# Kernel optimization log

Hardware: AMD Instinct MI355X
Metric: run time of the kernel (lower is better)

Reference implementation:

```python
import jax, jax.numpy as jnp
import numpy as np

B, S, D, H = 2, 2048, 1024, 16
DK = D // H  # 64


def setup_inputs() -> dict:
    key = jax.random.key(0)
    ks = jax.random.split(key, 9)
    query = jax.random.normal(ks[0], (B, S, D), dtype=jnp.float32)
    k_in = jax.random.normal(ks[1], (B, S, D), dtype=jnp.float32)
    v_in = jax.random.normal(ks[2], (B, S, D), dtype=jnp.float32)
    mask = jax.random.randint(ks[3], (B, S, S), 0, 2, dtype=jnp.int32)
    sc = 1.0 / np.sqrt(D)
    Wq = jax.random.normal(ks[4], (H, D, DK), dtype=jnp.float32) * sc  # per-head q proj
    Wk = jax.random.normal(ks[5], (H, D, DK), dtype=jnp.float32) * sc
    Wv = jax.random.normal(ks[6], (H, D, DK), dtype=jnp.float32) * sc
    Wu = jax.random.normal(ks[7], (D, D), dtype=jnp.float32) * sc  # unifyheads weight
    bu = jax.random.normal(ks[8], (D,), dtype=jnp.float32) * 0.01
    return {"query": query, "key": k_in, "value": v_in, "mask": mask,
            "Wq": Wq, "Wk": Wk, "Wv": Wv, "Wu": Wu, "bu": bu}


def reference(query, key, value, mask, Wq, Wk, Wv, Wu, bu):
    scale = DK ** 0.25  # original divides q and k each by d_k^(1/4)
    q = jnp.einsum('bsd,hdk->bhsk', query, Wq) / scale
    k = jnp.einsum('bsd,hdk->bhsk', key, Wk) / scale
    v = jnp.einsum('bsd,hdk->bhsk', value, Wv)
    scores = jnp.einsum('bhsk,bhtk->bhst', q, k)  # [B,H,S,S]
    scores = jnp.where(mask[:, None, :, :] == 0, jnp.float32(-1e9), scores)
    attn = jax.nn.softmax(scores, axis=-1)
    out = jnp.einsum('bhst,bhtk->bhsk', attn, v)
    out = jnp.transpose(out, (0, 2, 1, 3)).reshape(query.shape[0], query.shape[1], D)  # concat heads
    return out @ Wu + bu
```

## Files before the change

### kernel.cpp

```cpp
#include <hip/hip_runtime.h>
#include <hip/hip_bf16.h>


typedef __bf16 bf16_t;
typedef __attribute__((ext_vector_type(8))) __bf16 bf16x8;
typedef __attribute__((ext_vector_type(4))) float f32x4;
typedef unsigned int u32;

#define B_ 2
#define S_ 2048
#define D_ 1024
#define H_ 16
#define DK_ 64
#define NX_ (4096 * 1024)

static __device__ __forceinline__ f32x4 mfma16(bf16x8 a, bf16x8 b, f32x4 c) {
  return __builtin_amdgcn_mfma_f32_16x16x32_bf16(a, b, c, 0, 0, 0);
}

static __device__ __forceinline__ void async16(const bf16_t* g, bf16_t* l) {
  __builtin_amdgcn_global_load_lds(
      (const __attribute__((address_space(1))) u32*)g,
      (__attribute__((address_space(3))) u32*)l, 16, 0, 0);
}

__global__ __launch_bounds__(256) void cvt_x(const float* __restrict__ q,
                                             const float* __restrict__ k,
                                             const float* __restrict__ v,
                                             bf16_t* __restrict__ qo,
                                             bf16_t* __restrict__ ko,
                                             bf16_t* __restrict__ vo) {
  const int z = blockIdx.y;
  const float* src = (z == 0) ? q : (z == 1) ? k : v;
  bf16_t* dst = (z == 0) ? qo : (z == 1) ? ko : vo;
  size_t i = ((size_t)blockIdx.x * 256 + threadIdx.x) * 8;
  float4 a = *(const float4*)(src + i);
  float4 b = *(const float4*)(src + i + 4);
  bf16x8 o;
  o[0] = (bf16_t)a.x; o[1] = (bf16_t)a.y; o[2] = (bf16_t)a.z; o[3] = (bf16_t)a.w;
  o[4] = (bf16_t)b.x; o[5] = (bf16_t)b.y; o[6] = (bf16_t)b.z; o[7] = (bf16_t)b.w;
  *(bf16x8*)(dst + i) = o;
}

__global__ __launch_bounds__(256) void wtrans(
    const float* __restrict__ Wq, const float* __restrict__ Wk,
    const float* __restrict__ Wv, const float* __restrict__ Wu,
    bf16_t* __restrict__ Bq, bf16_t* __restrict__ Bk,
    bf16_t* __restrict__ Bv, bf16_t* __restrict__ Bu, float qkscale) {
  __shared__ __align__(16) bf16_t T[64][72];
  const int z = blockIdx.z;
  const float* W = (z == 0) ? Wq : (z == 1) ? Wk : (z == 2) ? Wv : Wu;
  bf16_t* BT = (z == 0) ? Bq : (z == 1) ? Bk : (z == 2) ? Bv : Bu;
  const float scale = (z <= 1) ? qkscale : 1.0f;
  const int d0 = blockIdx.x * 64, nt = blockIdx.y;
  const int tid = threadIdx.x;
  const int r = tid & 63, g = tid >> 6;

  const float* src = (z < 3)
      ? W + ((size_t)nt * D_ + d0 + r) * DK_ + g * 16
      : W + (size_t)(d0 + r) * D_ + nt * 64 + g * 16;
#pragma unroll
  for (int j = 0; j < 4; ++j) {
    float4 w4 = *(const float4*)(src + j * 4);
    T[g * 16 + j * 4 + 0][r] = (bf16_t)(w4.x * scale);
    T[g * 16 + j * 4 + 1][r] = (bf16_t)(w4.y * scale);
    T[g * 16 + j * 4 + 2][r] = (bf16_t)(w4.z * scale);
    T[g * 16 + j * 4 + 3][r] = (bf16_t)(w4.w * scale);
  }
  __syncthreads();
  const int orow = tid >> 3, seg = tid & 7;
#pragma unroll
  for (int p = 0; p < 2; ++p) {
    int rr = p * 32 + orow;
    *(bf16x8*)(BT + (size_t)(nt * 64 + rr) * D_ + d0 + seg * 8) =
        *(const bf16x8*)&T[rr][seg * 8];
  }
}

__global__ __launch_bounds__(256) void vt_build(const bf16_t* __restrict__ V,
                                                bf16_t* __restrict__ Vt) {
  __shared__ __align__(16) bf16_t T[64][72];
  const int r0 = blockIdx.x * 64;
  const int c0 = blockIdx.y * 64;
  const int tid = threadIdx.x;
#pragma unroll
  for (int it = 0; it < 2; ++it) {
    int t = tid + it * 256;
    int rr = t >> 3, cc = (t & 7) * 8;
    *(bf16x8*)&T[rr][cc] = *(const bf16x8*)(V + (size_t)(r0 + rr) * D_ + c0 + cc);
  }
  __syncthreads();
#pragma unroll
  for (int it = 0; it < 2; ++it) {
    int t = tid + it * 256;
    int cr = t >> 3, rc = (t & 7) * 8;
    bf16x8 v;
#pragma unroll
    for (int j = 0; j < 8; ++j) v[j] = T[rc + j][cr];
    *(bf16x8*)(Vt + (size_t)(c0 + cr) * 4096 + r0 + rc) = v;
  }
}

__global__ __launch_bounds__(256) void mask_pack(const int* __restrict__ mask,
                                                 unsigned int* __restrict__ bits) {
  int w = blockIdx.x * 256 + threadIdx.x;
  const int4* p = (const int4*)(mask + (size_t)w * 32);
  unsigned int v = 0;
#pragma unroll
  for (int i = 0; i < 8; ++i) {
    int4 m4 = p[i];
    v |= (m4.x != 0 ? 1u : 0u) << (i * 4 + 0);
    v |= (m4.y != 0 ? 1u : 0u) << (i * 4 + 1);
    v |= (m4.z != 0 ? 1u : 0u) << (i * 4 + 2);
    v |= (m4.w != 0 ? 1u : 0u) << (i * 4 + 3);
  }
  bits[w] = v;
}

template <bool BIAS_F32>
__global__ __launch_bounds__(256) void gemm_bt(
    const bf16_t* __restrict__ A0, const bf16_t* __restrict__ A1,
    const bf16_t* __restrict__ A2, const bf16_t* __restrict__ BT0,
    const bf16_t* __restrict__ BT1, const bf16_t* __restrict__ BT2,
    void* __restrict__ C0, void* __restrict__ C1, void* __restrict__ C2,
    const float* __restrict__ bias) {
  __shared__ __align__(16) bf16_t As[128 * 64];
  __shared__ __align__(16) bf16_t Bs[128 * 64];

  const int z = blockIdx.z;
  const bf16_t* A = (z == 0) ? A0 : (z == 1) ? A1 : A2;
  const bf16_t* BT = (z == 0) ? BT0 : (z == 1) ? BT1 : BT2;
  void* C = (z == 0) ? C0 : (z == 1) ? C1 : C2;

  const int tid = threadIdx.x;
  const int lane = tid & 63, wave = tid >> 6;
  const int l = lane & 15, quad = lane >> 4;
  const int wm = wave >> 1, wn = wave & 1;
  const int row0 = blockIdx.x * 128, col0 = blockIdx.y * 128;

  const int lr = lane >> 3;
  const int gc8 = (lane & 7) ^ lr;
  const int xl = l & 7;

  f32x4 acc[4][4];
#pragma unroll
  for (int i = 0; i < 4; ++i)
#pragma unroll
    for (int j = 0; j < 4; ++j) acc[i][j] = {0.f, 0.f, 0.f, 0.f};

  for (int k0 = 0; k0 < 1024; k0 += 64) {
    __syncthreads();
#pragma unroll
    for (int c = 0; c < 4; ++c) {
      int r = wave * 32 + c * 8;
      async16(A + (size_t)(row0 + r + lr) * 1024 + k0 + gc8 * 8, As + r * 64);
      async16(BT + (size_t)(col0 + r + lr) * 1024 + k0 + gc8 * 8, Bs + r * 64);
    }
    __syncthreads();

#pragma unroll
    for (int kh = 0; kh < 2; ++kh) {
      bf16x8 af[4], bf[4];
#pragma unroll
      for (int f = 0; f < 4; ++f)
        af[f] = *(const bf16x8*)&As[(wm * 64 + f * 16 + l) * 64 +
                                    (((kh * 4 + quad) ^ xl) * 8)];
#pragma unroll
      for (int f = 0; f < 4; ++f)
        bf[f] = *(const bf16x8*)&Bs[(wn * 64 + f * 16 + l) * 64 +
                                    (((kh * 4 + quad) ^ xl) * 8)];
#pragma unroll
      for (int fm = 0; fm < 4; ++fm)
#pragma unroll
        for (int fn = 0; fn < 4; ++fn)
          acc[fm][fn] = mfma16(af[fm], bf[fn], acc[fm][fn]);
    }
  }

#pragma unroll
  for (int fm = 0; fm < 4; ++fm)
#pragma unroll
    for (int fn = 0; fn < 4; ++fn)
#pragma unroll
      for (int reg = 0; reg < 4; ++reg) {
        int row = row0 + wm * 64 + fm * 16 + quad * 4 + reg;
        int col = col0 + wn * 64 + fn * 16 + l;
        if (BIAS_F32)
          ((float*)C)[(size_t)row * 1024 + col] = acc[fm][fn][reg] + bias[col];
        else
          ((bf16_t*)C)[(size_t)row * 1024 + col] = (bf16_t)acc[fm][fn][reg];
      }
}

__global__ __launch_bounds__(256) void attn_kernel(
    const bf16_t* __restrict__ Qx, const bf16_t* __restrict__ Kx,
    const bf16_t* __restrict__ Vt, const unsigned int* __restrict__ mbits,
    bf16_t* __restrict__ out) {
  __shared__ __align__(16) bf16_t Ks[64 * 64];
  __shared__ __align__(16) bf16_t Vts[64 * 64];
  __shared__ __align__(16) bf16_t Ps[4][32][72];

  const int tid = threadIdx.x;
  const int lane = tid & 63, wave = tid >> 6;
  const int l = lane & 15, quad = lane >> 4;
  const int qt = blockIdx.x, h = blockIdx.y, b = blockIdx.z;
  const int ch = h * 64;
  const size_t rb = (size_t)b * S_;
  const int q0 = qt * 128 + wave * 32;

  const int lr = lane >> 3;
  const int gc8 = (lane & 7) ^ lr;
  const int xl = l & 7;

  bf16x8 aq[2][2];
#pragma unroll
  for (int mf = 0; mf < 2; ++mf) {
    const bf16_t* qp = Qx + (rb + q0 + mf * 16 + l) * D_ + ch;
    aq[mf][0] = *(const bf16x8*)(qp + quad * 8);
    aq[mf][1] = *(const bf16x8*)(qp + 32 + quad * 8);
  }

  const f32x4 zero = {0.f, 0.f, 0.f, 0.f};
  f32x4 o[2][4];
  float lpart[2][4];
#pragma unroll
  for (int mf = 0; mf < 2; ++mf)
#pragma unroll
    for (int i = 0; i < 4; ++i) { o[mf][i] = zero; lpart[mf][i] = 0.f; }

  for (int t0 = 0; t0 < S_; t0 += 64) {
    __syncthreads();
#pragma unroll
    for (int it = 0; it < 2; ++it) {
      int r0 = it * 32 + wave * 8;
      async16(Kx + (rb + t0 + r0 + lr) * D_ + ch + gc8 * 8, Ks + r0 * 64);
      async16(Vt + (size_t)(ch + r0 + lr) * 4096 + rb + t0 + gc8 * 8,
              Vts + r0 * 64);
    }
    __syncthreads();

    f32x4 sf[2][4];
#pragma unroll
    for (int ts = 0; ts < 4; ++ts) {
      int rK = (ts * 16 + l) * 64;
      bf16x8 bk0 = *(const bf16x8*)&Ks[rK + ((quad ^ xl) * 8)];
      bf16x8 bk1 = *(const bf16x8*)&Ks[rK + (((4 + quad) ^ xl) * 8)];
#pragma unroll
      for (int mf = 0; mf < 2; ++mf) {
        f32x4 c = mfma16(aq[mf][0], bk0, zero);
        sf[mf][ts] = mfma16(aq[mf][1], bk1, c);
      }
    }

#pragma unroll
    for (int mf = 0; mf < 2; ++mf)
#pragma unroll
      for (int reg = 0; reg < 4; ++reg) {
        int srow = q0 + mf * 16 + quad * 4 + reg;
        const u32* mp = mbits + (size_t)(b * S_ + srow) * (S_ / 32) + (t0 >> 5);
        u32 w0 = mp[0], w1 = mp[1];
#pragma unroll
        for (int ts = 0; ts < 4; ++ts) {
          u32 w = (ts < 2) ? w0 : w1;
          int bit = (ts & 1) * 16 + l;
          float keep = (float)((w >> bit) & 1u);
          float p = __expf(fminf(sf[mf][ts][reg], 30.0f)) * keep;
          lpart[mf][reg] += p;
          Ps[wave][mf * 16 + quad * 4 + reg][ts * 16 + l] = (bf16_t)p;
        }
      }

    bf16x8 ap[2][2];
#pragma unroll
    for (int mf = 0; mf < 2; ++mf) {
      ap[mf][0] = *(const bf16x8*)&Ps[wave][mf * 16 + l][quad * 8];
      ap[mf][1] = *(const bf16x8*)&Ps[wave][mf * 16 + l][32 + quad * 8];
    }
#pragma unroll
    for (int nt = 0; nt < 4; ++nt) {
      int rV = (nt * 16 + l) * 64;
      bf16x8 bv0 = *(const bf16x8*)&Vts[rV + ((quad ^ xl) * 8)];
      bf16x8 bv1 = *(const bf16x8*)&Vts[rV + (((4 + quad) ^ xl) * 8)];
#pragma unroll
      for (int mf = 0; mf < 2; ++mf) {
        o[mf][nt] = mfma16(ap[mf][0], bv0, o[mf][nt]);
        o[mf][nt] = mfma16(ap[mf][1], bv1, o[mf][nt]);
      }
    }
  }

#pragma unroll
  for (int mf = 0; mf < 2; ++mf)
#pragma unroll
    for (int reg = 0; reg < 4; ++reg) {
      float rsum = lpart[mf][reg];
#pragma unroll
      for (int m = 1; m < 16; m <<= 1) rsum += __shfl_xor(rsum, m);
      float inv = (rsum > 0.f) ? (1.f / rsum) : 0.f;
      int srow = q0 + mf * 16 + quad * 4 + reg;
      bf16_t* op = out + (rb + srow) * D_ + ch;
#pragma unroll
      for (int nt = 0; nt < 4; ++nt)
        op[nt * 16 + l] = (bf16_t)(o[mf][nt][reg] * inv);
    }
}

extern "C" void kernel_launch(void* const* d_in, const int* in_sizes, int n_in,
                              void* d_out, int out_size, void* d_ws, size_t ws_size,
                              hipStream_t stream) {
  const float* q_in = (const float*)d_in[0];
  const float* k_in = (const float*)d_in[1];
  const float* v_in = (const float*)d_in[2];
  const int* mask = (const int*)d_in[3];
  const float* Wq = (const float*)d_in[4];
  const float* Wk = (const float*)d_in[5];
  const float* Wv = (const float*)d_in[6];
  const float* Wu = (const float*)d_in[7];
  const float* bu = (const float*)d_in[8];
  float* outp = (float*)d_out;

  bf16_t* qx = (bf16_t*)d_ws;
  bf16_t* kx = qx + NX_;
  bf16_t* vx = kx + NX_;
  bf16_t* qb = vx + NX_;
  bf16_t* kb = qb + NX_;
  bf16_t* vb = kb + NX_;
  bf16_t* BTq = vb + NX_;
  bf16_t* BTk = BTq + D_ * D_;
  bf16_t* BTv = BTk + D_ * D_;
  bf16_t* BTu = BTv + D_ * D_;
  unsigned int* mb = (unsigned int*)(BTu + D_ * D_);
  bf16_t* ab = qx;
  bf16_t* vtb = kx;

  const float qkscale = 0.35355339059327373f;

  dim3 blk(256);
  cvt_x<<<dim3(2048, 3), blk, 0, stream>>>(q_in, k_in, v_in, qx, kx, vx);
  wtrans<<<dim3(16, 16, 4), blk, 0, stream>>>(Wq, Wk, Wv, Wu, BTq, BTk, BTv, BTu, qkscale);
  mask_pack<<<dim3(1024), blk, 0, stream>>>(mask, mb);
  gemm_bt<false><<<dim3(32, 8, 3), blk, 0, stream>>>(qx, kx, vx, BTq, BTk, BTv,
                                                     qb, kb, vb, nullptr);
  vt_build<<<dim3(64, 16), blk, 0, stream>>>(vb, vtb);
  attn_kernel<<<dim3(S_ / 128, H_, B_), blk, 0, stream>>>(qb, kb, vtb, mb, ab);
  gemm_bt<true><<<dim3(32, 8, 1), blk, 0, stream>>>(ab, ab, ab, BTu, BTu, BTu,
                                                    outp, outp, outp, bu);
}
```

Baseline: 298.5 us.

## Transpose score MFMA, shrink attention blocks, use 64-row tiles for output GEMM

The attention kernel now computes S^T by swapping the MFMA operands, so each lane holds four consecutive keys for one query row. That lets it read one mask nibble per lane, write P to LDS as packed bf16x4, and keep one running sum per row group. Attention blocks drop to 128 threads covering 64 queries, doubling the grid to raise occupancy and CU coverage. The output projection gets its own 64x128-tile GEMM kernel, giving it twice as many blocks. The cost is more K/V tile reloads per query and smaller GEMM tiles with less reuse.

```diff
diff --git a/kernel.cpp b/kernel.cpp
--- a/kernel.cpp
+++ b/kernel.cpp
@@ -3,6 +3,7 @@
 
 
 typedef __bf16 bf16_t;
+typedef __attribute__((ext_vector_type(4))) __bf16 bf16x4;
 typedef __attribute__((ext_vector_type(8))) __bf16 bf16x8;
 typedef __attribute__((ext_vector_type(4))) float f32x4;
 typedef unsigned int u32;
@@ -117,20 +118,18 @@
   bits[w] = v;
 }
 
-template <bool BIAS_F32>
 __global__ __launch_bounds__(256) void gemm_bt(
     const bf16_t* __restrict__ A0, const bf16_t* __restrict__ A1,
     const bf16_t* __restrict__ A2, const bf16_t* __restrict__ BT0,
     const bf16_t* __restrict__ BT1, const bf16_t* __restrict__ BT2,
-    void* __restrict__ C0, void* __restrict__ C1, void* __restrict__ C2,
-    const float* __restrict__ bias) {
+    bf16_t* __restrict__ C0, bf16_t* __restrict__ C1, bf16_t* __restrict__ C2) {
   __shared__ __align__(16) bf16_t As[128 * 64];
   __shared__ __align__(16) bf16_t Bs[128 * 64];
 
   const int z = blockIdx.z;
   const bf16_t* A = (z == 0) ? A0 : (z == 1) ? A1 : A2;
   const bf16_t* BT = (z == 0) ? BT0 : (z == 1) ? BT1 : BT2;
-  void* C = (z == 0) ? C0 : (z == 1) ? C1 : C2;
+  bf16_t* C = (z == 0) ? C0 : (z == 1) ? C1 : C2;
 
   const int tid = threadIdx.x;
   const int lane = tid & 63, wave = tid >> 6;
@@ -185,20 +184,83 @@
       for (int reg = 0; reg < 4; ++reg) {
         int row = row0 + wm * 64 + fm * 16 + quad * 4 + reg;
         int col = col0 + wn * 64 + fn * 16 + l;
-        if (BIAS_F32)
-          ((float*)C)[(size_t)row * 1024 + col] = acc[fm][fn][reg] + bias[col];
-        else
-          ((bf16_t*)C)[(size_t)row * 1024 + col] = (bf16_t)acc[fm][fn][reg];
+        C[(size_t)row * 1024 + col] = (bf16_t)acc[fm][fn][reg];
       }
 }
 
-__global__ __launch_bounds__(256) void attn_kernel(
+__global__ __launch_bounds__(256) void gemm_bt64(
+    const bf16_t* __restrict__ A, const bf16_t* __restrict__ BT,
+    float* __restrict__ C, const float* __restrict__ bias) {
+  __shared__ __align__(16) bf16_t As[64 * 64];
+  __shared__ __align__(16) bf16_t Bs[128 * 64];
+
+  const int tid = threadIdx.x;
+  const int lane = tid & 63, wave = tid >> 6;
+  const int l = lane & 15, quad = lane >> 4;
+  const int row0 = blockIdx.x * 64, col0 = blockIdx.y * 128;
+
+  const int lr = lane >> 3;
+  const int gc8 = (lane & 7) ^ lr;
+  const int xl = l & 7;
+
+  f32x4 acc[4][2];
+#pragma unroll
+  for (int i = 0; i < 4; ++i)
+#pragma unroll
+    for (int j = 0; j < 2; ++j) acc[i][j] = {0.f, 0.f, 0.f, 0.f};
+
+  for (int k0 = 0; k0 < 1024; k0 += 64) {
+    __syncthreads();
+#pragma unroll
+    for (int c = 0; c < 2; ++c) {
+      int r = wave * 16 + c * 8;
+      async16(A + (size_t)(row0 + r + lr) * 1024 + k0 + gc8 * 8, As + r * 64);
+    }
+#pragma unroll
+    for (int c = 0; c < 4; ++c) {
+      int r = wave * 32 + c * 8;
+      async16(BT + (size_t)(col0 + r + lr) * 1024 + k0 + gc8 * 8, Bs + r * 64);
+    }
+    __syncthreads();
+
+#pragma unroll
+    for (int kh = 0; kh < 2; ++kh) {
+      bf16x8 af[4], bf[2];
+#pragma unroll
+      for (int f = 0; f < 4; ++f)
+        af[f] = *(const bf16x8*)&As[(f * 16 + l) * 64 +
+                                    (((kh * 4 + quad) ^ xl) * 8)];
+#pragma unroll
+      for (int f = 0; f < 2; ++f)
+        bf[f] = *(const bf16x8*)&Bs[(wave * 32 + f * 16 + l) * 64 +
+                                    (((kh * 4 + quad) ^ xl) * 8)];
+#pragma unroll
+      for (int fm = 0; fm < 4; ++fm)
+#pragma unroll
+        for (int fn = 0; fn < 2; ++fn)
+          acc[fm][fn] = mfma16(af[fm], bf[fn], acc[fm][fn]);
+    }
+  }
+
+#pragma unroll
+  for (int fm = 0; fm < 4; ++fm)
+#pragma unroll
+    for (int fn = 0; fn < 2; ++fn)
+#pragma unroll
+      for (int reg = 0; reg < 4; ++reg) {
+        int row = row0 + fm * 16 + quad * 4 + reg;
+        int col = col0 + wave * 32 + fn * 16 + l;
+        C[(size_t)row * 1024 + col] = acc[fm][fn][reg] + bias[col];
+      }
+}
+
+__global__ __launch_bounds__(128) void attn_kernel(
     const bf16_t* __restrict__ Qx, const bf16_t* __restrict__ Kx,
     const bf16_t* __restrict__ Vt, const unsigned int* __restrict__ mbits,
     bf16_t* __restrict__ out) {
   __shared__ __align__(16) bf16_t Ks[64 * 64];
   __shared__ __align__(16) bf16_t Vts[64 * 64];
-  __shared__ __align__(16) bf16_t Ps[4][32][72];
+  __shared__ __align__(16) bf16_t Ps[2][32][72];
 
   const int tid = threadIdx.x;
   const int lane = tid & 63, wave = tid >> 6;
@@ -206,69 +268,69 @@
   const int qt = blockIdx.x, h = blockIdx.y, b = blockIdx.z;
   const int ch = h * 64;
   const size_t rb = (size_t)b * S_;
-  const int q0 = qt * 128 + wave * 32;
+  const int q0 = qt * 64 + wave * 32;
 
   const int lr = lane >> 3;
   const int gc8 = (lane & 7) ^ lr;
   const int xl = l & 7;
 
-  bf16x8 aq[2][2];
+  bf16x8 bq[2][2];
 #pragma unroll
   for (int mf = 0; mf < 2; ++mf) {
     const bf16_t* qp = Qx + (rb + q0 + mf * 16 + l) * D_ + ch;
-    aq[mf][0] = *(const bf16x8*)(qp + quad * 8);
-    aq[mf][1] = *(const bf16x8*)(qp + 32 + quad * 8);
+    bq[mf][0] = *(const bf16x8*)(qp + quad * 8);
+    bq[mf][1] = *(const bf16x8*)(qp + 32 + quad * 8);
   }
 
   const f32x4 zero = {0.f, 0.f, 0.f, 0.f};
   f32x4 o[2][4];
-  float lpart[2][4];
+  float lsum[2] = {0.f, 0.f};
 #pragma unroll
   for (int mf = 0; mf < 2; ++mf)
 #pragma unroll
-    for (int i = 0; i < 4; ++i) { o[mf][i] = zero; lpart[mf][i] = 0.f; }
+    for (int nt = 0; nt < 4; ++nt) o[mf][nt] = zero;
+
+  const u32* mrow[2];
+#pragma unroll
+  for (int mf = 0; mf < 2; ++mf)
+    mrow[mf] = mbits + (size_t)(b * S_ + q0 + mf * 16 + l) * (S_ / 32);
 
   for (int t0 = 0; t0 < S_; t0 += 64) {
     __syncthreads();
 #pragma unroll
-    for (int it = 0; it < 2; ++it) {
-      int r0 = it * 32 + wave * 8;
+    for (int it = 0; it < 4; ++it) {
+      int r0 = it * 16 + wave * 8;
       async16(Kx + (rb + t0 + r0 + lr) * D_ + ch + gc8 * 8, Ks + r0 * 64);
       async16(Vt + (size_t)(ch + r0 + lr) * 4096 + rb + t0 + gc8 * 8,
               Vts + r0 * 64);
     }
     __syncthreads();
 
-    f32x4 sf[2][4];
-#pragma unroll
-    for (int ts = 0; ts < 4; ++ts) {
-      int rK = (ts * 16 + l) * 64;
-      bf16x8 bk0 = *(const bf16x8*)&Ks[rK + ((quad ^ xl) * 8)];
-      bf16x8 bk1 = *(const bf16x8*)&Ks[rK + (((4 + quad) ^ xl) * 8)];
-#pragma unroll
-      for (int mf = 0; mf < 2; ++mf) {
-        f32x4 c = mfma16(aq[mf][0], bk0, zero);
-        sf[mf][ts] = mfma16(aq[mf][1], bk1, c);
+#pragma unroll
+    for (int mf = 0; mf < 2; ++mf) {
+      u32 mw0 = mrow[mf][(t0 >> 5)];
+      u32 mw1 = mrow[mf][(t0 >> 5) + 1];
+#pragma unroll
+      for (int ts = 0; ts < 4; ++ts) {
+        int rK = (ts * 16 + l) * 64;
+        bf16x8 ak0 = *(const bf16x8*)&Ks[rK + ((quad ^ xl) * 8)];
+        bf16x8 ak1 = *(const bf16x8*)&Ks[rK + (((4 + quad) ^ xl) * 8)];
+        f32x4 s = mfma16(ak0, bq[mf][0], zero);
+        s = mfma16(ak1, bq[mf][1], s);
+
+        u32 mw = (ts < 2) ? mw0 : mw1;
+        u32 nib = (mw >> ((ts & 1) * 16 + quad * 4)) & 0xFu;
+        bf16x4 pv;
+#pragma unroll
+        for (int reg = 0; reg < 4; ++reg) {
+          float e = __expf(fminf(s[reg], 30.0f));
+          float p = ((nib >> reg) & 1u) ? e : 0.0f;
+          lsum[mf] += p;
+          pv[reg] = (bf16_t)p;
+        }
+        *(bf16x4*)&Ps[wave][mf * 16 + l][ts * 16 + quad * 4] = pv;
       }
     }
-
-#pragma unroll
-    for (int mf = 0; mf < 2; ++mf)
-#pragma unroll
-      for (int reg = 0; reg < 4; ++reg) {
-        int srow = q0 + mf * 16 + quad * 4 + reg;
-        const u32* mp = mbits + (size_t)(b * S_ + srow) * (S_ / 32) + (t0 >> 5);
-        u32 w0 = mp[0], w1 = mp[1];
-#pragma unroll
-        for (int ts = 0; ts < 4; ++ts) {
-          u32 w = (ts < 2) ? w0 : w1;
-          int bit = (ts & 1) * 16 + l;
-          float keep = (float)((w >> bit) & 1u);
-          float p = __expf(fminf(sf[mf][ts][reg], 30.0f)) * keep;
-          lpart[mf][reg] += p;
-          Ps[wave][mf * 16 + quad * 4 + reg][ts * 16 + l] = (bf16_t)p;
-        }
-      }
 
     bf16x8 ap[2][2];
 #pragma unroll
@@ -290,19 +352,23 @@
   }
 
 #pragma unroll
-  for (int mf = 0; mf < 2; ++mf)
+  for (int mf = 0; mf < 2; ++mf) {
+    float rsum = lsum[mf];
+    rsum += __shfl_xor(rsum, 16);
+    rsum += __shfl_xor(rsum, 32);
+    float inv = (rsum > 0.f) ? (1.f / rsum) : 0.f;
+    float invr[4];
+#pragma unroll
+    for (int reg = 0; reg < 4; ++reg) invr[reg] = __shfl(inv, quad * 4 + reg);
 #pragma unroll
     for (int reg = 0; reg < 4; ++reg) {
-      float rsum = lpart[mf][reg];
-#pragma unroll
-      for (int m = 1; m < 16; m <<= 1) rsum += __shfl_xor(rsum, m);
-      float inv = (rsum > 0.f) ? (1.f / rsum) : 0.f;
       int srow = q0 + mf * 16 + quad * 4 + reg;
       bf16_t* op = out + (rb + srow) * D_ + ch;
 #pragma unroll
       for (int nt = 0; nt < 4; ++nt)
-        op[nt * 16 + l] = (bf16_t)(o[mf][nt][reg] * inv);
-    }
+        op[nt * 16 + l] = (bf16_t)(o[mf][nt][reg] * invr[reg]);
+    }
+  }
 }
 
 extern "C" void kernel_launch(void* const* d_in, const int* in_sizes, int n_in,
@@ -339,10 +405,9 @@
   cvt_x<<<dim3(2048, 3), blk, 0, stream>>>(q_in, k_in, v_in, qx, kx, vx);
   wtrans<<<dim3(16, 16, 4), blk, 0, stream>>>(Wq, Wk, Wv, Wu, BTq, BTk, BTv, BTu, qkscale);
   mask_pack<<<dim3(1024), blk, 0, stream>>>(mask, mb);
-  gemm_bt<false><<<dim3(32, 8, 3), blk, 0, stream>>>(qx, kx, vx, BTq, BTk, BTv,
-                                                     qb, kb, vb, nullptr);
+  gemm_bt<<<dim3(32, 8, 3), blk, 0, stream>>>(qx, kx, vx, BTq, BTk, BTv,
+                                              qb, kb, vb);
   vt_build<<<dim3(64, 16), blk, 0, stream>>>(vb, vtb);
-  attn_kernel<<<dim3(S_ / 128, H_, B_), blk, 0, stream>>>(qb, kb, vtb, mb, ab);
-  gemm_bt<true><<<dim3(32, 8, 1), blk, 0, stream>>>(ab, ab, ab, BTu, BTu, BTu,
-                                                    outp, outp, outp, bu);
-}
+  attn_kernel<<<dim3(S_ / 64, H_, B_), dim3(128), 0, stream>>>(qb, kb, vtb, mb, ab);
+  gemm_bt64<<<dim3(64, 8), blk, 0, stream>>>(ab, BTu, outp, bu);
+}
```

Result: faster. 287.3 us (-3.8%).
